# Kernel optimization log

Measured on AMD Instinct MI355X. Metric: run time of the kernel, lower is better.

The kernel has to match this reference:

```python
import jax, jax.numpy as jnp
import numpy as np

B, N, E = 4, 8192, 2048          # batch, nodes, hyperedges
IN_CH, OUT_CH = 64, 64
P_EDGE = 0.05                    # incidence density


def setup_inputs() -> dict:
    key = jax.random.key(0)
    kx, kh, kt = jax.random.split(key, 3)
    x = jax.random.normal(kx, (B, N, IN_CH), dtype=jnp.float32)
    # sparse 0/1 incidence matrix; p=0.05 guarantees nonzero degrees w.h.p.
    H = (jax.random.uniform(kh, (B, N, E)) < P_EDGE).astype(jnp.float32)
    theta = jax.random.normal(kt, (IN_CH, OUT_CH), dtype=jnp.float32) * (1.0 / np.sqrt(IN_CH))
    bias = jnp.zeros((OUT_CH,), dtype=jnp.float32)
    return {"x": x, "H": H, "theta": theta, "bias": bias}


def reference(x, H, theta, bias):
    # x: [B,N,Cin], H: [B,N,E] incidence, theta: [Cin,Cout], bias: [Cout]
    x = jnp.einsum('bni,io->bno', x, theta)          # feature transform
    # hyperedge features: (H^T x) / deg_e  -- replaces diag(deg)^-1 matmul
    deg_e = jnp.sum(H, axis=1)                       # [B,E]
    xe = jnp.einsum('bne,bno->beo', H, x) / deg_e[:, :, None]
    # node features: (H xe) / deg_n
    deg_n = jnp.sum(H, axis=2)                       # [B,N]
    xn = jnp.einsum('bne,beo->bno', H, xe) / deg_n[:, :, None]
    return xn + bias
```

## Files before the change

### kernel.cpp

```cpp
#include <hip/hip_runtime.h>
#include <stdint.h>

#define NB 4
#define NN 8192
#define NE 2048
#define NC 64
#define KS2 8
#define NW8 (NN / 8)
#define EW8 (NE / 8)

typedef __bf16 bf16x8 __attribute__((ext_vector_type(8)));
typedef float f32x16 __attribute__((ext_vector_type(16)));
typedef unsigned long long u64;

__device__ __forceinline__ unsigned short f2bf(float f) {
  union { float f; uint32_t u; } v; v.f = f;
  return (unsigned short)((v.u + 0x7FFFu + ((v.u >> 16) & 1u)) >> 16);
}
__device__ __forceinline__ bf16x8 ld_bf8(const void* p) { return *(const bf16x8*)p; }

__device__ __forceinline__ u64 bt_step(u64 x, int k, u64 M1, int lane) {
  const u64 y = (u64)__shfl_xor((long long)x, k, 64);
  const u64 M0 = ~M1;
  return ((lane & k) == 0) ? ((x & M0) | ((y & M0) << k))
                           : ((x & M1) | ((y >> k) & M0));
}
__device__ __forceinline__ u64 bit_transpose64(u64 x, int lane) {
  x = bt_step(x, 1,  0xAAAAAAAAAAAAAAAAull, lane);
  x = bt_step(x, 2,  0xCCCCCCCCCCCCCCCCull, lane);
  x = bt_step(x, 4,  0xF0F0F0F0F0F0F0F0ull, lane);
  x = bt_step(x, 8,  0xFF00FF00FF00FF00ull, lane);
  x = bt_step(x, 16, 0xFFFF0000FFFF0000ull, lane);
  x = bt_step(x, 32, 0xFFFFFFFF00000000ull, lane);
  return x;
}

#define LUT_INIT(lut)                                                     \
  {                                                                       \
    union { uint32_t u[4]; uint4 v; } e_;                                 \
    const uint32_t by_ = threadIdx.x & 255;                               \
    _Pragma("unroll")                                                     \
    for (int p_ = 0; p_ < 4; ++p_) {                                      \
      const uint32_t t_ = (by_ >> (2 * p_)) & 3u;                         \
      e_.u[p_] = (t_ & 1u) * 0x3F80u + (t_ & 2u) * 0x1FC00000u;           \
    }                                                                     \
    lut[by_] = e_.v;                                                      \
  }

__global__ __launch_bounds__(256) void k_transform(
    const float* __restrict__ x, const float* __restrict__ theta,
    unsigned short* __restrict__ xt_blk) {
  const int b = blockIdx.y, ns = blockIdx.x;
  const int n0 = ns * 64;
  __shared__ float xs[64][65];
  __shared__ float th[64][64];
  const int tid = threadIdx.x, w = tid >> 6, l = tid & 63;
  for (int k = tid; k < 4096; k += 256) th[k >> 6][k & 63] = theta[k];
  const float* xrow = x + ((size_t)b * NN + n0) * NC;
  for (int k = tid; k < 4096; k += 256) xs[k >> 6][k & 63] = xrow[k];
  __syncthreads();
  float acc[16];
  #pragma unroll
  for (int j = 0; j < 16; ++j) acc[j] = 0.f;
  #pragma unroll 4
  for (int i = 0; i < 64; ++i) {
    const float xv = xs[l][i];
    const float4* t4 = (const float4*)(&th[i][w * 16]);
    const float4 a0 = t4[0], a1 = t4[1], a2 = t4[2], a3 = t4[3];
    acc[0]  += xv * a0.x; acc[1]  += xv * a0.y; acc[2]  += xv * a0.z; acc[3]  += xv * a0.w;
    acc[4]  += xv * a1.x; acc[5]  += xv * a1.y; acc[6]  += xv * a1.z; acc[7]  += xv * a1.w;
    acc[8]  += xv * a2.x; acc[9]  += xv * a2.y; acc[10] += xv * a2.z; acc[11] += xv * a2.w;
    acc[12] += xv * a3.x; acc[13] += xv * a3.y; acc[14] += xv * a3.z; acc[15] += xv * a3.w;
  }
  __syncthreads();
  unsigned short* ost = (unsigned short*)&xs[0][0];
  #pragma unroll
  for (int j = 0; j < 16; ++j) ost[l * 64 + w * 16 + j] = f2bf(acc[j]);
  __syncthreads();
  unsigned short* obase = xt_blk + ((size_t)b * NW8 + ns * 8) * 512;
  for (int c = tid; c < 512; c += 256) {
    const int g = c >> 6, o = c & 63;
    union { unsigned short s[8]; uint4 v; } pk;
    #pragma unroll
    for (int k = 0; k < 8; ++k) pk.s[k] = ost[(g * 8 + k) * 64 + o];
    *(uint4*)(obase + (size_t)c * 8) = pk.v;
  }
}

__global__ __launch_bounds__(256) void k_pack(
    const float* __restrict__ H, u64* __restrict__ bitsN,
    u64* __restrict__ bitsE) {
  const int ns = blockIdx.x >> 2, eh = blockIdx.x & 3, b = blockIdx.y;
  const int w = threadIdx.x >> 6, l = threadIdx.x & 63;
  const int n0 = ns * 64;
  const int strip = eh * 4 + w;
  const float* Hb = H + ((size_t)b * NN + n0) * NE + strip * 128 + 2 * l;
  u64* bn = bitsN + ((size_t)b * 128 + ns) * NE + strip * 128 + 2 * l;
  u64* be = bitsE + (size_t)b * 32 * NN + n0 + l;
  const u64 top = 0x8000000000000000ull;

  u64 wn0 = 0, wn1 = 0;
  float2 pf[8];
  #pragma unroll
  for (int j = 0; j < 8; ++j) pf[j] = *(const float2*)(Hb + (size_t)j * NE);
  #pragma unroll 8
  for (int r = 0; r < 56; ++r) {
    const float2 v = pf[r & 7];
    pf[r & 7] = *(const float2*)(Hb + (size_t)(r + 8) * NE);
    wn0 = (wn0 >> 1) | (v.x != 0.f ? top : 0);
    wn1 = (wn1 >> 1) | (v.y != 0.f ? top : 0);
  }
  #pragma unroll
  for (int r = 56; r < 64; ++r) {
    const float2 v = pf[r & 7];
    wn0 = (wn0 >> 1) | (v.x != 0.f ? top : 0);
    wn1 = (wn1 >> 1) | (v.y != 0.f ? top : 0);
  }
  *(ulonglong2*)bn = make_ulonglong2(wn0, wn1);
  be[(size_t)(strip * 2 + 0) * NN] = bit_transpose64(wn0, l);
  be[(size_t)(strip * 2 + 1) * NN] = bit_transpose64(wn1, l);
}

__global__ __launch_bounds__(256) void k_edge2(
    const u64* __restrict__ bitsN, const unsigned short* __restrict__ xt_blk,
    float* __restrict__ xe_part, float* __restrict__ deg_part) {
  const int ew = blockIdx.x, b = blockIdx.y, ks = blockIdx.z;
  const int tid = threadIdx.x, w = tid >> 6, l = tid & 63, q = l >> 5;
  __shared__ uint4 lut[256];
  LUT_INIT(lut)
  __syncthreads();
  const int erow = (w & 1) * 32 + (l & 31);
  const int ocol = (w >> 1) * 32 + (l & 31);
  const int enat = (ew >> 1) * 128 + 2 * erow + (ew & 1);
  const u64* Nb = bitsN + ((size_t)b * 128 + ks * 16) * NE + enat;
  const unsigned short* Bb =
      xt_blk + ((size_t)b * NW8 + ks * 128) * 512 + (size_t)ocol * 8;
  float* xo = xe_part + ((size_t)(ks * NB + b)) * (NE * NC) +
              (size_t)ew * 64 * NC + ocol;

  u64 wb[16];
  #pragma unroll
  for (int nt = 0; nt < 16; ++nt) wb[nt] = Nb[(size_t)nt * NE];

  f32x16 acc;
  #pragma unroll
  for (int j = 0; j < 16; ++j) acc[j] = 0.f;
  int dcount = 0;
  #pragma unroll
  for (int nt = 0; nt < 16; ++nt) {
    const u64 wbits = wb[nt];
    dcount += __popcll(wbits);
    #pragma unroll
    for (int kk = 0; kk < 4; ++kk) {
      const bf16x8 av =
          *(const bf16x8*)&lut[(uint32_t)(wbits >> (8 * (kk * 2 + q))) & 0xFFu];
      const bf16x8 bv = ld_bf8(Bb + (size_t)(nt * 8 + kk * 2 + q) * 512);
      acc = __builtin_amdgcn_mfma_f32_32x32x16_bf16(av, bv, acc, 0, 0, 0);
    }
  }
  #pragma unroll
  for (int r = 0; r < 16; ++r) {
    const int rho = (w & 1) * 32 + 4 * q + (r & 3) + 8 * (r >> 2);
    xo[(size_t)rho * NC] = acc[r];
  }
  if (w < 2 && q == 0)
    deg_part[(size_t)(ks * NB + b) * NE + ew * 64 + erow] = (float)dcount;
}

__global__ __launch_bounds__(256) void k_edge_norm(
    const float* __restrict__ xe_part, const float* __restrict__ deg_part,
    unsigned short* __restrict__ xe_blk) {
  const int eb = blockIdx.x, b = blockIdx.y, tid = threadIdx.x;
  __shared__ unsigned short tt[64][72];
  __shared__ float dinv[64];
  if (tid < 64) {
    float s = 0.f;
    #pragma unroll
    for (int ks = 0; ks < KS2; ++ks)
      s += deg_part[(size_t)ks * (NB * NE) + b * NE + eb * 64 + tid];
    dinv[tid] = s > 0.f ? 1.0f / s : 0.f;
  }
  __syncthreads();
  const int o = tid & 63, eg = tid >> 6;
  #pragma unroll 4
  for (int j = 0; j < 16; ++j) {
    const int el = eg * 16 + j;
    const size_t idx = ((size_t)b * NE + eb * 64 + el) * NC + o;
    float s = 0.f;
    #pragma unroll
    for (int ks = 0; ks < KS2; ++ks) s += xe_part[(size_t)ks * (NB * NE * NC) + idx];
    tt[el][o] = f2bf(s * dinv[el]);
  }
  __syncthreads();
  unsigned short* obase = xe_blk + ((size_t)b * EW8 + eb * 8) * 512;
  for (int c = tid; c < 512; c += 256) {
    const int g = c >> 6, oo = c & 63;
    union { unsigned short s[8]; uint4 v; } pk;
    #pragma unroll
    for (int k = 0; k < 8; ++k) pk.s[k] = tt[g * 8 + k][oo];
    *(uint4*)(obase + (size_t)c * 8) = pk.v;
  }
}

__global__ __launch_bounds__(256) void k_node2(
    const u64* __restrict__ bitsE, const unsigned short* __restrict__ xe_blk,
    const float* __restrict__ bias, float* __restrict__ out) {
  const int ns = blockIdx.x, b = blockIdx.y;
  const int n0 = ns * 64;
  const int tid = threadIdx.x, w = tid >> 6, l = tid & 63, q = l >> 5;
  __shared__ uint4 lut[256];
  __shared__ float ldsDeg[64];
  LUT_INIT(lut)
  const int arow = (w & 1) * 32 + (l & 31);
  const int ocol = (w >> 1) * 32 + (l & 31);
  const u64* Eb = bitsE + (size_t)b * 32 * NN + n0 + arow;
  const unsigned short* Bb = xe_blk + (size_t)b * EW8 * 512 + (size_t)ocol * 8;
  __syncthreads();

  u64 wb[32];
  #pragma unroll
  for (int et = 0; et < 32; ++et) wb[et] = Eb[(size_t)et * NN];

  f32x16 acc;
  #pragma unroll
  for (int j = 0; j < 16; ++j) acc[j] = 0.f;
  int dcount = 0;
  #pragma unroll
  for (int et = 0; et < 32; ++et) {
    const u64 wbits = wb[et];
    dcount += __popcll(wbits);
    #pragma unroll
    for (int kk = 0; kk < 4; ++kk) {
      const bf16x8 av =
          *(const bf16x8*)&lut[(uint32_t)(wbits >> (8 * (kk * 2 + q))) & 0xFFu];
      const bf16x8 bv = ld_bf8(Bb + (size_t)(et * 8 + kk * 2 + q) * 512);
      acc = __builtin_amdgcn_mfma_f32_32x32x16_bf16(av, bv, acc, 0, 0, 0);
    }
  }
  if (w < 2 && q == 0) ldsDeg[arow] = dcount > 0 ? 1.0f / (float)dcount : 0.f;
  __syncthreads();
  const float bv0 = bias[ocol];
  #pragma unroll
  for (int r = 0; r < 16; ++r) {
    const int rho = (w & 1) * 32 + 4 * q + (r & 3) + 8 * (r >> 2);
    out[((size_t)b * NN + n0 + rho) * NC + ocol] = acc[r] * ldsDeg[rho] + bv0;
  }
}

extern "C" void kernel_launch(void* const* d_in, const int* in_sizes, int n_in,
                              void* d_out, int out_size, void* d_ws, size_t ws_size,
                              hipStream_t stream) {
  const float* x     = (const float*)d_in[0];
  const float* H     = (const float*)d_in[1];
  const float* theta = (const float*)d_in[2];
  const float* bias  = (const float*)d_in[3];
  float* out = (float*)d_out;
  char* ws = (char*)d_ws;

  unsigned short* xt_blk = (unsigned short*)ws;
  u64* bitsN             = (u64*)(ws + (4ull << 20));
  u64* bitsE             = (u64*)(ws + (12ull << 20));
  float* xe_part         = (float*)(ws + (20ull << 20));
  float* deg_part        = (float*)(ws + (36ull << 20));
  unsigned short* xe_blk = (unsigned short*)(ws + (37ull << 20));

  k_transform<<<dim3(NN / 64, NB), 256, 0, stream>>>(x, theta, xt_blk);
  k_pack<<<dim3((NN / 64) * 4, NB), 256, 0, stream>>>(H, bitsN, bitsE);
  k_edge2<<<dim3(32, NB, KS2), 256, 0, stream>>>(bitsN, xt_blk, xe_part, deg_part);
  k_edge_norm<<<dim3(NE / 64, NB), 256, 0, stream>>>(xe_part, deg_part, xe_blk);
  k_node2<<<dim3(NN / 64, NB), 256, 0, stream>>>(bitsE, xe_blk, bias, out);
}
```

Measured before the change: 99.64 us.

## Compute two edge tiles per block in edge kernel and deepen K-split

Each k_edge2 block now handles 128 hyperedges with two MFMA accumulators that share every loaded B fragment, and reads the incidence bits as 128-bit vector loads. This halves the B-operand traffic per edge. When the workspace is large enough, the K-split goes from 8 to 16 so the grid still has 256 blocks. The deeper split makes the partial-sum buffer twice as large, which raises the traffic and reduction work in k_edge_norm.

```diff
diff --git a/kernel.cpp b/kernel.cpp
--- a/kernel.cpp
+++ b/kernel.cpp
@@ -5,7 +5,6 @@
 #define NN 8192
 #define NE 2048
 #define NC 64
-#define KS2 8
 #define NW8 (NN / 8)
 #define EW8 (NE / 8)
 
@@ -121,52 +120,61 @@
   be[(size_t)(strip * 2 + 1) * NN] = bit_transpose64(wn1, l);
 }
 
+template <int KS>
 __global__ __launch_bounds__(256) void k_edge2(
     const u64* __restrict__ bitsN, const unsigned short* __restrict__ xt_blk,
     float* __restrict__ xe_part, float* __restrict__ deg_part) {
-  const int ew = blockIdx.x, b = blockIdx.y, ks = blockIdx.z;
+  constexpr int NT = 128 / KS;
+  const int ewp = blockIdx.x, b = blockIdx.y, ks = blockIdx.z;
   const int tid = threadIdx.x, w = tid >> 6, l = tid & 63, q = l >> 5;
   __shared__ uint4 lut[256];
   LUT_INIT(lut)
   __syncthreads();
   const int erow = (w & 1) * 32 + (l & 31);
   const int ocol = (w >> 1) * 32 + (l & 31);
-  const int enat = (ew >> 1) * 128 + 2 * erow + (ew & 1);
-  const u64* Nb = bitsN + ((size_t)b * 128 + ks * 16) * NE + enat;
+  const u64* Nb = bitsN + ((size_t)b * 128 + ks * NT) * NE + ewp * 128 + 2 * erow;
   const unsigned short* Bb =
-      xt_blk + ((size_t)b * NW8 + ks * 128) * 512 + (size_t)ocol * 8;
-  float* xo = xe_part + ((size_t)(ks * NB + b)) * (NE * NC) +
-              (size_t)ew * 64 * NC + ocol;
-
-  u64 wb[16];
-  #pragma unroll
-  for (int nt = 0; nt < 16; ++nt) wb[nt] = Nb[(size_t)nt * NE];
-
-  f32x16 acc;
-  #pragma unroll
-  for (int j = 0; j < 16; ++j) acc[j] = 0.f;
-  int dcount = 0;
-  #pragma unroll
-  for (int nt = 0; nt < 16; ++nt) {
-    const u64 wbits = wb[nt];
-    dcount += __popcll(wbits);
+      xt_blk + ((size_t)b * NW8 + ks * (NT * 8)) * 512 + (size_t)ocol * 8;
+
+  ulonglong2 wb[NT];
+  #pragma unroll
+  for (int nt = 0; nt < NT; ++nt)
+    wb[nt] = *(const ulonglong2*)(Nb + (size_t)nt * NE);
+
+  f32x16 acc0, acc1;
+  #pragma unroll
+  for (int j = 0; j < 16; ++j) { acc0[j] = 0.f; acc1[j] = 0.f; }
+  int dc0 = 0, dc1 = 0;
+  #pragma unroll
+  for (int nt = 0; nt < NT; ++nt) {
+    const u64 w0 = wb[nt].x, w1 = wb[nt].y;
+    dc0 += __popcll(w0); dc1 += __popcll(w1);
     #pragma unroll
     for (int kk = 0; kk < 4; ++kk) {
-      const bf16x8 av =
-          *(const bf16x8*)&lut[(uint32_t)(wbits >> (8 * (kk * 2 + q))) & 0xFFu];
       const bf16x8 bv = ld_bf8(Bb + (size_t)(nt * 8 + kk * 2 + q) * 512);
-      acc = __builtin_amdgcn_mfma_f32_32x32x16_bf16(av, bv, acc, 0, 0, 0);
+      const bf16x8 av0 =
+          *(const bf16x8*)&lut[(uint32_t)(w0 >> (8 * (kk * 2 + q))) & 0xFFu];
+      const bf16x8 av1 =
+          *(const bf16x8*)&lut[(uint32_t)(w1 >> (8 * (kk * 2 + q))) & 0xFFu];
+      acc0 = __builtin_amdgcn_mfma_f32_32x32x16_bf16(av0, bv, acc0, 0, 0, 0);
+      acc1 = __builtin_amdgcn_mfma_f32_32x32x16_bf16(av1, bv, acc1, 0, 0, 0);
     }
   }
+  float* xo0 = xe_part + ((size_t)(ks * NB + b)) * (NE * NC) +
+               (size_t)(ewp * 128) * NC + ocol;
   #pragma unroll
   for (int r = 0; r < 16; ++r) {
     const int rho = (w & 1) * 32 + 4 * q + (r & 3) + 8 * (r >> 2);
-    xo[(size_t)rho * NC] = acc[r];
-  }
-  if (w < 2 && q == 0)
-    deg_part[(size_t)(ks * NB + b) * NE + ew * 64 + erow] = (float)dcount;
-}
-
+    xo0[(size_t)rho * NC] = acc0[r];
+    xo0[(size_t)(rho + 64) * NC] = acc1[r];
+  }
+  if (w < 2 && q == 0) {
+    deg_part[(size_t)(ks * NB + b) * NE + ewp * 128 + erow] = (float)dc0;
+    deg_part[(size_t)(ks * NB + b) * NE + ewp * 128 + 64 + erow] = (float)dc1;
+  }
+}
+
+template <int KS>
 __global__ __launch_bounds__(256) void k_edge_norm(
     const float* __restrict__ xe_part, const float* __restrict__ deg_part,
     unsigned short* __restrict__ xe_blk) {
@@ -176,7 +184,7 @@
   if (tid < 64) {
     float s = 0.f;
     #pragma unroll
-    for (int ks = 0; ks < KS2; ++ks)
+    for (int ks = 0; ks < KS; ++ks)
       s += deg_part[(size_t)ks * (NB * NE) + b * NE + eb * 64 + tid];
     dinv[tid] = s > 0.f ? 1.0f / s : 0.f;
   }
@@ -188,7 +196,7 @@
     const size_t idx = ((size_t)b * NE + eb * 64 + el) * NC + o;
     float s = 0.f;
     #pragma unroll
-    for (int ks = 0; ks < KS2; ++ks) s += xe_part[(size_t)ks * (NB * NE * NC) + idx];
+    for (int ks = 0; ks < KS; ++ks) s += xe_part[(size_t)ks * (NB * NE * NC) + idx];
     tt[el][o] = f2bf(s * dinv[el]);
   }
   __syncthreads();
@@ -261,12 +269,21 @@
   u64* bitsN             = (u64*)(ws + (4ull << 20));
   u64* bitsE             = (u64*)(ws + (12ull << 20));
   float* xe_part         = (float*)(ws + (20ull << 20));
-  float* deg_part        = (float*)(ws + (36ull << 20));
-  unsigned short* xe_blk = (unsigned short*)(ws + (37ull << 20));
 
   k_transform<<<dim3(NN / 64, NB), 256, 0, stream>>>(x, theta, xt_blk);
   k_pack<<<dim3((NN / 64) * 4, NB), 256, 0, stream>>>(H, bitsN, bitsE);
-  k_edge2<<<dim3(32, NB, KS2), 256, 0, stream>>>(bitsN, xt_blk, xe_part, deg_part);
-  k_edge_norm<<<dim3(NE / 64, NB), 256, 0, stream>>>(xe_part, deg_part, xe_blk);
-  k_node2<<<dim3(NN / 64, NB), 256, 0, stream>>>(bitsE, xe_blk, bias, out);
-}
+
+  if (ws_size >= (54ull << 20)) {
+    float* deg_part        = (float*)(ws + (52ull << 20));
+    unsigned short* xe_blk = (unsigned short*)(ws + (53ull << 20));
+    k_edge2<16><<<dim3(16, NB, 16), 256, 0, stream>>>(bitsN, xt_blk, xe_part, deg_part);
+    k_edge_norm<16><<<dim3(NE / 64, NB), 256, 0, stream>>>(xe_part, deg_part, xe_blk);
+    k_node2<<<dim3(NN / 64, NB), 256, 0, stream>>>(bitsE, xe_blk, bias, out);
+  } else {
+    float* deg_part        = (float*)(ws + (36ull << 20));
+    unsigned short* xe_blk = (unsigned short*)(ws + (37ull << 20));
+    k_edge2<8><<<dim3(16, NB, 8), 256, 0, stream>>>(bitsN, xt_blk, xe_part, deg_part);
+    k_edge_norm<8><<<dim3(NE / 64, NB), 256, 0, stream>>>(xe_part, deg_part, xe_blk);
+    k_node2<<<dim3(NN / 64, NB), 256, 0, stream>>>(bitsE, xe_blk, bias, out);
+  }
+}
```

After: 136.5 us. 37.0% more time.
